# Kernel tuning notes

Measured on AMD Instinct MI355X. Metric: run time of the kernel, lower is better.

The kernel has to match this reference:

```python
import jax, jax.numpy as jnp
import numpy as np
from jax import lax

NDEMOG, IC, OC, KS = 4, 128, 256, 3
B, H, W = 64, 56, 56


def setup_inputs() -> dict:
    key = jax.random.key(0)
    k1, k2, k3, k4 = jax.random.split(key, 4)
    x = jax.random.normal(k1, (B, IC, H, W), dtype=jnp.float32)
    demog_label = jax.random.randint(k2, (B,), 0, NDEMOG, dtype=jnp.int32)
    kernel_base = jax.random.normal(k3, (OC, IC, KS, KS), dtype=jnp.float32) * 0.05
    kernel_mask = jax.random.uniform(k4, (NDEMOG, IC, KS, KS), dtype=jnp.float32)
    return {"x": x, "demog_label": demog_label, "kernel_base": kernel_base,
            "kernel_mask": kernel_mask, "epoch": 5}


def _conv(x, k):
    # NCHW / OIHW, stride=1, padding=1 (same as F.conv2d(stride=1, padding=1))
    return lax.conv_general_dilated(
        x, k, window_strides=(1, 1), padding=[(1, 1), (1, 1)],
        dimension_numbers=("NCHW", "OIHW", "NCHW"))


def reference(x, demog_label, kernel_base, kernel_mask, epoch):
    # epoch (=5) < fuse_epoch (=9) in the original module, so the per-demographic
    # mask kernel_mask[d] is always used. The torch code gathers the samples of
    # each demographic group, convolves with kernel_base * mask[d], and scatters
    # results back. Equivalent fused form: conv the full batch with each masked
    # kernel and select per-sample by demog_label (ndemog is a small constant).
    ndemog = kernel_mask.shape[0]
    out = jnp.zeros((x.shape[0], kernel_base.shape[0], x.shape[2], x.shape[3]), x.dtype)
    for d in range(ndemog):
        k = kernel_base * kernel_mask[d][None]          # [OC, IC, KS, KS]
        y = _conv(x, k)                                  # [B, OC, H, W]
        sel = (demog_label == d)[:, None, None, None]
        out = out + jnp.where(sel, y, jnp.zeros((), x.dtype))
    return out
```

## Files before the change

### kernel.cpp

```cpp
#include <hip/hip_runtime.h>


typedef __bf16 v8bf __attribute__((ext_vector_type(8)));
typedef float  v4f  __attribute__((ext_vector_type(4)));
typedef unsigned short v8us __attribute__((ext_vector_type(8)));

#define IC_  128
#define OC_  256
#define HH   56
#define WW_  56
#define HW_  3136
#define PW   58
#define XP_PER_B (PW * PW * IC_)
#define WQ_ELEMS (4 * 9 * OC_ * IC_)

__device__ __forceinline__ unsigned short f2bf(float f) {
    unsigned u = __builtin_bit_cast(unsigned, f);
    u += 0x7fffu + ((u >> 16) & 1u);
    return (unsigned short)(u >> 16);
}

typedef __attribute__((address_space(3))) unsigned int lds_u32_t;
typedef const __attribute__((address_space(1))) unsigned int gbl_u32_t;

__device__ __forceinline__ void gload_lds16(const unsigned short* gsrc, unsigned short* ldst) {
    __builtin_amdgcn_global_load_lds((gbl_u32_t*)gsrc,
                                     (lds_u32_t*)(unsigned int)(unsigned long long)(uintptr_t)ldst,
                                     16, 0, 0);
}

__global__ __launch_bounds__(256)
void transpose_pad(const float* __restrict__ x, unsigned short* __restrict__ xp)
{
    __shared__ unsigned short lt[IC_ * 60];
    const int blk = blockIdx.x;
    const int b = blk / HH, h = blk % HH;
    const int t = threadIdx.x;
    const float* xb = x + (size_t)b * IC_ * HW_ + h * WW_;
    #pragma unroll
    for (int i = 0; i < 28; ++i) {
        int e  = t + i * 256;
        int ic = e / WW_;
        int w  = e - ic * WW_;
        lt[ic * 60 + w] = f2bf(xb[ic * HW_ + w]);
    }
    __syncthreads();
    unsigned short* xpb = xp + (size_t)b * XP_PER_B + (size_t)(h + 1) * PW * IC_;
    #pragma unroll
    for (int i = 0; i < 4; ++i) {
        int s = t + i * 256;
        if (s < 896) {
            int w = s >> 4, icg = s & 15;
            unsigned short v[8];
            #pragma unroll
            for (int j = 0; j < 8; ++j) v[j] = lt[(icg * 8 + j) * 60 + w];
            *(v8us*)&xpb[(w + 1) * IC_ + icg * 8] = *(const v8us*)v;
        }
    }
}

__global__ __launch_bounds__(256)
void build_weights(const float* __restrict__ kbase, const float* __restrict__ kmask,
                   unsigned short* __restrict__ wq)
{
    int t  = blockIdx.x * 256 + threadIdx.x;
    int ic = t & 127;
    int oc = (t >> 7) & 255;
    int rd = t >> 15;
    int r  = rd % 9, d = rd / 9;
    float v = kbase[oc * 1152 + ic * 9 + r] * kmask[d * 1152 + ic * 9 + r];
    wq[t] = f2bf(v);
}

__global__ __launch_bounds__(256)
void adaconv_main(const unsigned short* __restrict__ xp,
                  const unsigned short* __restrict__ wq,
                  const int* __restrict__ demog,
                  float* __restrict__ out)
{
    __shared__ unsigned short lds_a[64 * 32];
    __shared__ unsigned short lds_b[256 * 32];

    const int t    = threadIdx.x;
    const int lane = t & 63;
    const int quad = lane >> 4;
    const int l15  = lane & 15;
    const int wid  = __builtin_amdgcn_readfirstlane(t >> 6);

    const int mtile = blockIdx.x;
    const int b     = blockIdx.y;
    const int p0    = mtile * 64;
    const int d     = demog[b];

    const int spix = p0 + (t >> 2);
    const int sh   = spix / WW_;
    const int sw   = spix - sh * WW_;
    const unsigned short* asrc = xp + (size_t)b * XP_PER_B
                               + (size_t)((sh + 1) * PW + (sw + 1)) * IC_ + (t & 3) * 8;
    const unsigned short* bsrc = wq + (size_t)d * 9 * OC_ * IC_
                               + (t >> 2) * IC_ + (t & 3) * 8;

    unsigned short* lda_dst = lds_a + wid * 512;
    unsigned short* ldb_dst = lds_b + wid * 512;

    v4f acc[4][4];
    #pragma unroll
    for (int mi = 0; mi < 4; ++mi)
        #pragma unroll
        for (int ni = 0; ni < 4; ++ni)
            acc[mi][ni] = (v4f)0.0f;

    #pragma unroll
    for (int r = 0; r < 9; ++r) {
        const int toff = ((r / 3 - 1) * PW + (r % 3 - 1)) * IC_;
        #pragma unroll
        for (int icb = 0; icb < 4; ++icb) {
            const int ic0 = icb * 32;
            __syncthreads();
            gload_lds16(asrc + toff + ic0, lda_dst);
            #pragma unroll
            for (int j = 0; j < 4; ++j)
                gload_lds16(bsrc + r * (OC_ * IC_) + j * 64 * IC_ + ic0,
                            ldb_dst + j * 2048);
            __syncthreads();

            v8us au[4], bu[4];
            #pragma unroll
            for (int mi = 0; mi < 4; ++mi)
                au[mi] = *(const v8us*)&lds_a[(mi * 16 + l15) * 32 + quad * 8];
            #pragma unroll
            for (int ni = 0; ni < 4; ++ni)
                bu[ni] = *(const v8us*)&lds_b[(wid * 64 + ni * 16 + l15) * 32 + quad * 8];

            #pragma unroll
            for (int mi = 0; mi < 4; ++mi) {
                v8bf a = __builtin_bit_cast(v8bf, au[mi]);
                #pragma unroll
                for (int ni = 0; ni < 4; ++ni) {
                    v8bf bb = __builtin_bit_cast(v8bf, bu[ni]);
                    acc[mi][ni] = __builtin_amdgcn_mfma_f32_16x16x32_bf16(a, bb, acc[mi][ni], 0, 0, 0);
                }
            }
        }
    }

    float* ob = out + ((size_t)b * OC_ + wid * 64) * HW_ + p0;
    #pragma unroll
    for (int ni = 0; ni < 4; ++ni) {
        #pragma unroll
        for (int mi = 0; mi < 4; ++mi) {
            float* o = ob + (size_t)(ni * 16 + l15) * HW_ + mi * 16 + quad * 4;
            *(v4f*)o = acc[mi][ni];
        }
    }
}

extern "C" void kernel_launch(void* const* d_in, const int* in_sizes, int n_in,
                              void* d_out, int out_size, void* d_ws, size_t ws_size,
                              hipStream_t stream) {
    const float* x     = (const float*)d_in[0];
    const int*   demog = (const int*)d_in[1];
    const float* kbase = (const float*)d_in[2];
    const float* kmask = (const float*)d_in[3];
    float* out = (float*)d_out;

    unsigned short* xp = (unsigned short*)d_ws;
    unsigned short* wq = xp + (size_t)64 * XP_PER_B;
    hipMemsetAsync(d_ws, 0, (size_t)64 * XP_PER_B * sizeof(unsigned short), stream);
    transpose_pad<<<64 * HH, 256, 0, stream>>>(x, xp);
    build_weights<<<WQ_ELEMS / 256, 256, 0, stream>>>(kbase, kmask, wq);
    adaconv_main<<<dim3(49, 64), 256, 0, stream>>>(xp, wq, demog, out);
}
```

Before: 451.0 us.

## Double-buffer LDS loads in conv GEMM and drop full-buffer memset for border zeroing

The main conv kernel now double-buffers the A and B tiles in LDS: it issues async global-to-LDS loads for the next chunk while running MFMAs on the current one, with one barrier per chunk instead of two. The separate memset of the whole padded input buffer is replaced by having the transpose kernel zero only the padding columns and the top and bottom padding rows. The transpose also reads four floats per load instead of one. This doubles LDS use per block and adds a launch-bounds occupancy hint.

```diff
diff --git a/kernel.cpp b/kernel.cpp
--- a/kernel.cpp
+++ b/kernel.cpp
@@ -32,17 +32,22 @@
 __global__ __launch_bounds__(256)
 void transpose_pad(const float* __restrict__ x, unsigned short* __restrict__ xp)
 {
-    __shared__ unsigned short lt[IC_ * 60];
+    __shared__ unsigned short lt[IC_ * 58];
     const int blk = blockIdx.x;
     const int b = blk / HH, h = blk % HH;
     const int t = threadIdx.x;
     const float* xb = x + (size_t)b * IC_ * HW_ + h * WW_;
     #pragma unroll
-    for (int i = 0; i < 28; ++i) {
-        int e  = t + i * 256;
-        int ic = e / WW_;
-        int w  = e - ic * WW_;
-        lt[ic * 60 + w] = f2bf(xb[ic * HW_ + w]);
+    for (int i = 0; i < 7; ++i) {
+        int e4 = t + i * 256;
+        int ic = e4 / 14;
+        int w4 = (e4 - ic * 14) * 4;
+        v4f v = *(const v4f*)&xb[ic * HW_ + w4];
+        unsigned lo = (unsigned)f2bf(v[0]) | ((unsigned)f2bf(v[1]) << 16);
+        unsigned hi = (unsigned)f2bf(v[2]) | ((unsigned)f2bf(v[3]) << 16);
+        unsigned* dst = (unsigned*)&lt[ic * 58 + w4];
+        dst[0] = lo;
+        dst[1] = hi;
     }
     __syncthreads();
     unsigned short* xpb = xp + (size_t)b * XP_PER_B + (size_t)(h + 1) * PW * IC_;
@@ -53,9 +58,18 @@
             int w = s >> 4, icg = s & 15;
             unsigned short v[8];
             #pragma unroll
-            for (int j = 0; j < 8; ++j) v[j] = lt[(icg * 8 + j) * 60 + w];
+            for (int j = 0; j < 8; ++j) v[j] = lt[(icg * 8 + j) * 58 + w];
             *(v8us*)&xpb[(w + 1) * IC_ + icg * 8] = *(const v8us*)v;
         }
+    }
+    if (t < 32) {
+        int col = (t >> 4) * 57;
+        *(v8us*)&xpb[(size_t)col * IC_ + (t & 15) * 8] = (v8us)(unsigned short)0;
+    }
+    if (h == 0 || h == HH - 1) {
+        unsigned short* row = xp + (size_t)b * XP_PER_B + (h == 0 ? 0 : (size_t)(PW - 1) * PW * IC_);
+        for (int s = t; s < 928; s += 256)
+            *(v8us*)&row[(size_t)s * 8] = (v8us)(unsigned short)0;
     }
 }
 
@@ -72,14 +86,14 @@
     wq[t] = f2bf(v);
 }
 
-__global__ __launch_bounds__(256)
+__global__ __launch_bounds__(256, 4)
 void adaconv_main(const unsigned short* __restrict__ xp,
                   const unsigned short* __restrict__ wq,
                   const int* __restrict__ demog,
                   float* __restrict__ out)
 {
-    __shared__ unsigned short lds_a[64 * 32];
-    __shared__ unsigned short lds_b[256 * 32];
+    __shared__ unsigned short lds_a[2][64 * 32];
+    __shared__ unsigned short lds_b[2][256 * 32];
 
     const int t    = threadIdx.x;
     const int lane = t & 63;
@@ -100,9 +114,6 @@
     const unsigned short* bsrc = wq + (size_t)d * 9 * OC_ * IC_
                                + (t >> 2) * IC_ + (t & 3) * 8;
 
-    unsigned short* lda_dst = lds_a + wid * 512;
-    unsigned short* ldb_dst = lds_b + wid * 512;
-
     v4f acc[4][4];
     #pragma unroll
     for (int mi = 0; mi < 4; ++mi)
@@ -110,39 +121,47 @@
         for (int ni = 0; ni < 4; ++ni)
             acc[mi][ni] = (v4f)0.0f;
 
+    #define STAGE(buf, c)                                                              \
+        do {                                                                           \
+            const int r_   = (c) >> 2;                                                 \
+            const int icb_ = (c) & 3;                                                  \
+            const int toff_ = ((r_ / 3 - 1) * PW + (r_ % 3 - 1)) * IC_;                \
+            const int ic0_  = icb_ * 32;                                               \
+            gload_lds16(asrc + toff_ + ic0_, &lds_a[(buf)][wid * 512]);                \
+            _Pragma("unroll")                                                          \
+            for (int j = 0; j < 4; ++j)                                                \
+                gload_lds16(bsrc + r_ * (OC_ * IC_) + j * 64 * IC_ + ic0_,             \
+                            &lds_b[(buf)][wid * 512 + j * 2048]);                      \
+        } while (0)
+
+    STAGE(0, 0);
+    __syncthreads();
+
     #pragma unroll
-    for (int r = 0; r < 9; ++r) {
-        const int toff = ((r / 3 - 1) * PW + (r % 3 - 1)) * IC_;
+    for (int c = 0; c < 36; ++c) {
+        const int cur = c & 1;
+        if (c + 1 < 36) STAGE(cur ^ 1, c + 1);
+
+        v8us au[4], bu[4];
         #pragma unroll
-        for (int icb = 0; icb < 4; ++icb) {
-            const int ic0 = icb * 32;
-            __syncthreads();
-            gload_lds16(asrc + toff + ic0, lda_dst);
+        for (int mi = 0; mi < 4; ++mi)
+            au[mi] = *(const v8us*)&lds_a[cur][(mi * 16 + l15) * 32 + quad * 8];
+        #pragma unroll
+        for (int ni = 0; ni < 4; ++ni)
+            bu[ni] = *(const v8us*)&lds_b[cur][(wid * 64 + ni * 16 + l15) * 32 + quad * 8];
+
+        #pragma unroll
+        for (int mi = 0; mi < 4; ++mi) {
+            v8bf a = __builtin_bit_cast(v8bf, au[mi]);
             #pragma unroll
-            for (int j = 0; j < 4; ++j)
-                gload_lds16(bsrc + r * (OC_ * IC_) + j * 64 * IC_ + ic0,
-                            ldb_dst + j * 2048);
-            __syncthreads();
-
-            v8us au[4], bu[4];
-            #pragma unroll
-            for (int mi = 0; mi < 4; ++mi)
-                au[mi] = *(const v8us*)&lds_a[(mi * 16 + l15) * 32 + quad * 8];
-            #pragma unroll
-            for (int ni = 0; ni < 4; ++ni)
-                bu[ni] = *(const v8us*)&lds_b[(wid * 64 + ni * 16 + l15) * 32 + quad * 8];
-
-            #pragma unroll
-            for (int mi = 0; mi < 4; ++mi) {
-                v8bf a = __builtin_bit_cast(v8bf, au[mi]);
-                #pragma unroll
-                for (int ni = 0; ni < 4; ++ni) {
-                    v8bf bb = __builtin_bit_cast(v8bf, bu[ni]);
-                    acc[mi][ni] = __builtin_amdgcn_mfma_f32_16x16x32_bf16(a, bb, acc[mi][ni], 0, 0, 0);
-                }
+            for (int ni = 0; ni < 4; ++ni) {
+                v8bf bb = __builtin_bit_cast(v8bf, bu[ni]);
+                acc[mi][ni] = __builtin_amdgcn_mfma_f32_16x16x32_bf16(a, bb, acc[mi][ni], 0, 0, 0);
             }
         }
+        __syncthreads();
     }
+    #undef STAGE
 
     float* ob = out + ((size_t)b * OC_ + wid * 64) * HW_ + p0;
     #pragma unroll
@@ -166,7 +185,6 @@
 
     unsigned short* xp = (unsigned short*)d_ws;
     unsigned short* wq = xp + (size_t)64 * XP_PER_B;
-    hipMemsetAsync(d_ws, 0, (size_t)64 * XP_PER_B * sizeof(unsigned short), stream);
     transpose_pad<<<64 * HH, 256, 0, stream>>>(x, xp);
     build_weights<<<WQ_ELEMS / 256, 256, 0, stream>>>(kbase, kmask, wq);
     adaconv_main<<<dim3(49, 64), 256, 0, stream>>>(xp, wq, demog, out);
```

New measurement: 449.5 us. Within noise of the previous version (-0.3%).
